# Kernel tuning notes

Measured on AMD Instinct MI355X. Metric: run time of the kernel, lower is better.

The kernel has to match this reference:

```python
import jax, jax.numpy as jnp
import numpy as np

D_MODEL, D_FF, D_NEURON, N_HEADS = 1024, 4096, 128, 8
HEAD_DIM = D_NEURON // N_HEADS
LN_EPS = 1e-5

def gelu(x):
    return jax.nn.gelu(x, approximate=False)  # torch default is exact erf GELU

def setup_inputs() -> dict:
    key = jax.random.key(0)
    ks = jax.random.split(key, 16)
    s = 0.02
    inp = {
        "x": jax.random.normal(ks[0], (2, 2048, D_MODEL), jnp.float32),
        "neuron_patterns": jax.random.normal(ks[1], (D_FF, D_MODEL), jnp.float32) * s,
        "neuron_vecs": jax.random.normal(ks[2], (D_FF, D_NEURON), jnp.float32) * s,
        "neuron_out_dirs": jax.random.normal(ks[3], (D_FF, D_MODEL), jnp.float32) * s,
        "router_w1": jax.random.normal(ks[4], (D_MODEL, D_MODEL), jnp.float32) * s,
        "router_w2": jax.random.normal(ks[5], (D_FF, D_MODEL), jnp.float32) * s,
        "ln_g": jnp.ones((D_MODEL,), jnp.float32),
        "ln_b": jnp.zeros((D_MODEL,), jnp.float32),
        "in_proj_w": jax.random.normal(ks[6], (3 * D_NEURON, D_NEURON), jnp.float32) * s,
        "in_proj_b": jnp.zeros((3 * D_NEURON,), jnp.float32),
        "out_proj_w": jax.random.normal(ks[7], (D_NEURON, D_NEURON), jnp.float32) * s,
        "out_proj_b": jnp.zeros((D_NEURON,), jnp.float32),
        "wp1_w": jax.random.normal(ks[8], (D_NEURON // 2, D_NEURON), jnp.float32) * s,
        "wp1_b": jnp.zeros((D_NEURON // 2,), jnp.float32),
        "wp2_w": jax.random.normal(ks[9], (1, D_NEURON // 2), jnp.float32) * s,
        "wp2_b": jnp.zeros((1,), jnp.float32),
        "top_k": 32,
    }
    return inp

def _forward(x, neuron_patterns, neuron_vecs, neuron_out_dirs, router_w1, router_w2,
             ln_g, ln_b, in_proj_w, in_proj_b, out_proj_w, out_proj_b,
             wp1_w, wp1_b, wp2_w, wp2_b, top_k):
    B, S, D = x.shape
    xf = x.reshape(-1, D)                                  # [N, D]
    # Router (MLP): LayerNorm -> gelu(x @ W1^T) -> @ W2^T
    mu = jnp.mean(xf, axis=-1, keepdims=True)
    var = jnp.mean(jnp.square(xf - mu), axis=-1, keepdims=True)
    xn = (xf - mu) * jax.lax.rsqrt(var + LN_EPS) * ln_g + ln_b
    h = gelu(xn @ router_w1.T)
    scores = h @ router_w2.T                               # [N, d_ff]
    _, idx = jax.lax.top_k(scores, top_k)                  # [N, k]
    pats = neuron_patterns[idx]                            # [N, k, D]
    sems = neuron_vecs[idx]                                # [N, k, dn]
    dirs = neuron_out_dirs[idx]                            # [N, k, D]
    base = gelu(jnp.einsum('nd,nkd->nk', xf, pats))        # [N, k]
    # Small self-attention over the k gathered neuron semantics (eval: no dropout)
    qkv = sems @ in_proj_w.T + in_proj_b                   # [N, k, 3*dn]
    q, kk, v = jnp.split(qkv, 3, axis=-1)
    N, K = q.shape[0], q.shape[1]
    q = q.reshape(N, K, N_HEADS, HEAD_DIM)
    kk = kk.reshape(N, K, N_HEADS, HEAD_DIM)
    v = v.reshape(N, K, N_HEADS, HEAD_DIM)
    att = jnp.einsum('nqhd,nkhd->nhqk', q, kk) / jnp.sqrt(jnp.float32(HEAD_DIM))
    att = jax.nn.softmax(att, axis=-1)
    ao = jnp.einsum('nhqk,nkhd->nqhd', att, v).reshape(N, K, D_NEURON)
    attended = ao @ out_proj_w.T + out_proj_b              # [N, k, dn]
    # Gate: sigmoid(MLP(attended)) -> [N, k, 1]
    sw = jax.nn.sigmoid(gelu(attended @ wp1_w.T + wp1_b) @ wp2_w.T + wp2_b)
    final = base[..., None] * sw                           # [N, k, 1]
    out = jnp.einsum('nko,nkd->nd', final, dirs)           # sum over k neurons
    return out.reshape(B, S, D)

def reference(x, neuron_patterns, neuron_vecs, neuron_out_dirs, router_w1, router_w2,
              ln_g, ln_b, in_proj_w, in_proj_b, out_proj_w, out_proj_b,
              wp1_w, wp1_b, wp2_w, wp2_b, top_k):
    return _forward(x, neuron_patterns, neuron_vecs, neuron_out_dirs, router_w1, router_w2,
                    ln_g, ln_b, in_proj_w, in_proj_b, out_proj_w, out_proj_b,
                    wp1_w, wp1_b, wp2_w, wp2_b, top_k)
```

## Files before the change

### kernel.cpp

```cpp
#include <hip/hip_runtime.h>
#include <math.h>

#define N_TOK 4096
#define DM 1024
#define DFF 4096
#define DN 128
#define NH 8
#define HD 16
#define KSEL 32
#define KCAND 48
#define KMAX 64

typedef __attribute__((ext_vector_type(4))) float floatx4;
typedef __attribute__((ext_vector_type(8))) short short8;
typedef __attribute__((ext_vector_type(8))) unsigned short ushort8v;
typedef __attribute__((ext_vector_type(4))) unsigned short ushort4v;

__device__ __forceinline__ float gelu_f(float x) {
  return 0.5f * x * (1.0f + erff(x * 0.70710678118654752440f));
}
__device__ __forceinline__ float bf2f(unsigned short u) {
  union { unsigned int i; float f; } v; v.i = ((unsigned int)u) << 16; return v.f;
}
__device__ __forceinline__ unsigned short f2bf(float f) {
  unsigned int x = __float_as_uint(f);
  unsigned int r = (x + 0x7fffu + ((x >> 16) & 1u)) >> 16;
  return (unsigned short)r;
}
__device__ __forceinline__ void split3(float v, unsigned short& h, unsigned short& m,
                                       unsigned short& lo) {
  h = f2bf(v);
  float r1 = v - bf2f(h);
  m = f2bf(r1);
  float r2 = r1 - bf2f(m);
  lo = f2bf(r2);
}

__global__ __launch_bounds__(256) void ln3_kernel(const float* __restrict__ x,
    const float* __restrict__ g, const float* __restrict__ b,
    unsigned short* __restrict__ xh, unsigned short* __restrict__ xm,
    unsigned short* __restrict__ xl) {
  int n = blockIdx.x, tid = threadIdx.x;
  const float* row = x + (size_t)n * DM;
  float s = 0.f, sq = 0.f;
  for (int i = tid; i < DM; i += 256) { float v = row[i]; s += v; sq += v * v; }
  for (int off = 32; off; off >>= 1) { s += __shfl_down(s, off); sq += __shfl_down(sq, off); }
  __shared__ float ss[4], ssq[4];
  __shared__ float s_mu, s_rs;
  int wid = tid >> 6;
  if ((tid & 63) == 0) { ss[wid] = s; ssq[wid] = sq; }
  __syncthreads();
  if (tid == 0) {
    float S = ss[0] + ss[1] + ss[2] + ss[3];
    float Q = ssq[0] + ssq[1] + ssq[2] + ssq[3];
    float mu = S * (1.f / DM);
    float var = Q * (1.f / DM) - mu * mu;
    s_mu = mu; s_rs = rsqrtf(var + 1e-5f);
  }
  __syncthreads();
  float mu = s_mu, rs = s_rs;
  size_t base = (size_t)n * DM;
  for (int i = tid; i < DM; i += 256) {
    float v = (row[i] - mu) * rs * g[i] + b[i];
    unsigned short h, m, lo;
    split3(v, h, m, lo);
    xh[base + i] = h; xm[base + i] = m; xl[base + i] = lo;
  }
}

__global__ __launch_bounds__(256) void prep_kernel(
    const float* __restrict__ rw2, unsigned short* __restrict__ w2b,
    const float* __restrict__ pats, unsigned short* __restrict__ patsb,
    const float* __restrict__ dirs, unsigned short* __restrict__ dirsb,
    const float* __restrict__ opw, unsigned short* __restrict__ opwb,
    const float* __restrict__ w1, unsigned short* __restrict__ w1b,
    const float* __restrict__ rw1, unsigned short* __restrict__ w1h,
    unsigned short* __restrict__ w1m, unsigned short* __restrict__ w1l) {
  int b = blockIdx.x, t = threadIdx.x;
  if (b < 12288) {
    const float* src; unsigned short* dst; int local;
    if (b < 4096) { src = rw2; dst = w2b; local = b; }
    else if (b < 8192) { src = pats; dst = patsb; local = b - 4096; }
    else { src = dirs; dst = dirsb; local = b - 8192; }
    int i = (local * 256 + t) * 4;
    float4 v = *(const float4*)(src + i);
    ushort4v o = {f2bf(v.x), f2bf(v.y), f2bf(v.z), f2bf(v.w)};
    *(ushort4v*)(dst + i) = o;
  } else if (b < 12304) {
    int i = ((b - 12288) * 256 + t) * 4;
    float4 v = *(const float4*)(opw + i);
    ushort4v o = {f2bf(v.x), f2bf(v.y), f2bf(v.z), f2bf(v.w)};
    *(ushort4v*)(opwb + i) = o;
  } else if (b < 12312) {
    int i = ((b - 12304) * 256 + t) * 4;
    float4 v = *(const float4*)(w1 + i);
    ushort4v o = {f2bf(v.x), f2bf(v.y), f2bf(v.z), f2bf(v.w)};
    *(ushort4v*)(w1b + i) = o;
  } else {
    int i = ((b - 12312) * 256 + t) * 4;
    float4 v = *(const float4*)(rw1 + i);
    unsigned short h0, m0, l0, h1, m1, l1, h2, m2, l2, h3, m3, l3;
    split3(v.x, h0, m0, l0);
    split3(v.y, h1, m1, l1);
    split3(v.z, h2, m2, l2);
    split3(v.w, h3, m3, l3);
    ushort4v hh = {h0, h1, h2, h3};
    ushort4v mm = {m0, m1, m2, m3};
    ushort4v ll = {l0, l1, l2, l3};
    *(ushort4v*)(w1h + i) = hh;
    *(ushort4v*)(w1m + i) = mm;
    *(ushort4v*)(w1l + i) = ll;
  }
}

__global__ __launch_bounds__(256) void gemm1s(
    const unsigned short* __restrict__ Ah_, const unsigned short* __restrict__ Am_,
    const unsigned short* __restrict__ Al_, const unsigned short* __restrict__ Bh_,
    const unsigned short* __restrict__ Bm_, const unsigned short* __restrict__ Bl_,
    float* __restrict__ H, unsigned short* __restrict__ Hb) {
  __shared__ short Ahs[64 * 32], Ams[64 * 32], Als[64 * 32];
  __shared__ short Bhs[64 * 32], Bms[64 * 32], Bls[64 * 32];
  const int K = 1024;
  const int N = DM;
  int tid = threadIdx.x;
  int w = tid >> 6, l = tid & 63;
  int wr = w >> 1, wc = w & 1;
  size_t brow = (size_t)blockIdx.y * 64;
  size_t bcol = (size_t)blockIdx.x * 64;

  int r0 = w * 16 + (l >> 2);
  int g0 = (l & 3) ^ ((r0 >> 1) & 3);
  size_t oA = (brow + r0) * (size_t)K + g0 * 8;
  size_t oB = (bcol + r0) * (size_t)K + g0 * 8;
  const short* gAh = (const short*)Ah_ + oA;
  const short* gAm = (const short*)Am_ + oA;
  const short* gAl = (const short*)Al_ + oA;
  const short* gBh = (const short*)Bh_ + oB;
  const short* gBm = (const short*)Bm_ + oB;
  const short* gBl = (const short*)Bl_ + oB;
  short* lAh = &Ahs[w * 512]; short* lAm = &Ams[w * 512]; short* lAl = &Als[w * 512];
  short* lBh = &Bhs[w * 512]; short* lBm = &Bms[w * 512]; short* lBl = &Bls[w * 512];

  const short8 *pah[2], *pam[2], *pal[2], *pbh[2], *pbm[2], *pbl[2];
#pragma unroll
  for (int i = 0; i < 2; i++) {
    int m = wr * 32 + i * 16 + (l & 15);
    int slot = m * 4 + ((l >> 4) ^ ((m >> 1) & 3));
    pah[i] = (const short8*)&Ahs[slot * 8];
    pam[i] = (const short8*)&Ams[slot * 8];
    pal[i] = (const short8*)&Als[slot * 8];
    int nn = wc * 32 + i * 16 + (l & 15);
    int slotb = nn * 4 + ((l >> 4) ^ ((nn >> 1) & 3));
    pbh[i] = (const short8*)&Bhs[slotb * 8];
    pbm[i] = (const short8*)&Bms[slotb * 8];
    pbl[i] = (const short8*)&Bls[slotb * 8];
  }

  floatx4 acc[2][2];
#pragma unroll
  for (int i = 0; i < 2; i++)
#pragma unroll
    for (int j = 0; j < 2; j++) acc[i][j] = (floatx4){0.f, 0.f, 0.f, 0.f};

#define GLD(GP, LB) \
  __builtin_amdgcn_global_load_lds((const __attribute__((address_space(1))) unsigned int*)(GP), \
                                   (__attribute__((address_space(3))) unsigned int*)(LB), 16, 0, 0)

  for (int k0 = 0; k0 < K; k0 += 32) {
    __syncthreads();
    GLD(gAh + k0, lAh); GLD(gAm + k0, lAm); GLD(gAl + k0, lAl);
    GLD(gBh + k0, lBh); GLD(gBm + k0, lBm); GLD(gBl + k0, lBl);
    __syncthreads();
    short8 ah[2], am[2], al[2], bh[2], bm[2], bl[2];
#pragma unroll
    for (int i = 0; i < 2; i++) {
      ah[i] = *pah[i]; am[i] = *pam[i]; al[i] = *pal[i];
      bh[i] = *pbh[i]; bm[i] = *pbm[i]; bl[i] = *pbl[i];
    }
#pragma unroll
    for (int i = 0; i < 2; i++)
#pragma unroll
      for (int j = 0; j < 2; j++)
        acc[i][j] = __builtin_amdgcn_mfma_f32_16x16x32_bf16(ah[i], bh[j], acc[i][j], 0, 0, 0);
#pragma unroll
    for (int i = 0; i < 2; i++)
#pragma unroll
      for (int j = 0; j < 2; j++)
        acc[i][j] = __builtin_amdgcn_mfma_f32_16x16x32_bf16(am[i], bh[j], acc[i][j], 0, 0, 0);
#pragma unroll
    for (int i = 0; i < 2; i++)
#pragma unroll
      for (int j = 0; j < 2; j++)
        acc[i][j] = __builtin_amdgcn_mfma_f32_16x16x32_bf16(ah[i], bm[j], acc[i][j], 0, 0, 0);
#pragma unroll
    for (int i = 0; i < 2; i++)
#pragma unroll
      for (int j = 0; j < 2; j++)
        acc[i][j] = __builtin_amdgcn_mfma_f32_16x16x32_bf16(al[i], bh[j], acc[i][j], 0, 0, 0);
#pragma unroll
    for (int i = 0; i < 2; i++)
#pragma unroll
      for (int j = 0; j < 2; j++)
        acc[i][j] = __builtin_amdgcn_mfma_f32_16x16x32_bf16(ah[i], bl[j], acc[i][j], 0, 0, 0);
#pragma unroll
    for (int i = 0; i < 2; i++)
#pragma unroll
      for (int j = 0; j < 2; j++)
        acc[i][j] = __builtin_amdgcn_mfma_f32_16x16x32_bf16(am[i], bm[j], acc[i][j], 0, 0, 0);
  }
#undef GLD

#pragma unroll
  for (int i = 0; i < 2; i++) {
#pragma unroll
    for (int j = 0; j < 2; j++) {
#pragma unroll
      for (int r = 0; r < 4; r++) {
        size_t row = brow + wr * 32 + i * 16 + (l >> 4) * 4 + r;
        size_t col = bcol + wc * 32 + j * 16 + (l & 15);
        float v = gelu_f(acc[i][j][r]);
        H[row * N + col] = v;
        Hb[row * N + col] = f2bf(v);
      }
    }
  }
}

__global__ __launch_bounds__(256) void gemm_bf(const unsigned short* __restrict__ Ah,
    const unsigned short* __restrict__ Bh, unsigned short* __restrict__ C) {
  __shared__ short Asd[128 * 32];
  __shared__ short Bsd[128 * 32];
  const int K = 1024;
  int tid = threadIdx.x;
  int w = tid >> 6, l = tid & 63;
  size_t brow = (size_t)blockIdx.y * 128;
  size_t bcol = (size_t)blockIdx.x * 128;
  const short* Ab = (const short*)Ah + brow * K;
  const short* Bb = (const short*)Bh + bcol * K;

  int r0 = w * 32 + (l >> 2);
  int g0 = (l & 3) ^ ((r0 >> 1) & 3);
  const short* Ag0 = Ab + (size_t)r0 * K + g0 * 8;
  const short* Ag1 = Ab + (size_t)(r0 + 16) * K + g0 * 8;
  const short* Bg0 = Bb + (size_t)r0 * K + g0 * 8;
  const short* Bg1 = Bb + (size_t)(r0 + 16) * K + g0 * 8;
  short* ALds0 = &Asd[w * 1024];
  short* ALds1 = &Asd[w * 1024 + 512];
  short* BLds0 = &Bsd[w * 1024];
  short* BLds1 = &Bsd[w * 1024 + 512];

  const short8* aptr[4];
  const short8* bptr[4];
#pragma unroll
  for (int i = 0; i < 4; i++) {
    int m = (w >> 1) * 64 + i * 16 + (l & 15);
    int slot = m * 4 + ((l >> 4) ^ ((m >> 1) & 3));
    aptr[i] = (const short8*)&Asd[slot * 8];
    int n = (w & 1) * 64 + i * 16 + (l & 15);
    int slotb = n * 4 + ((l >> 4) ^ ((n >> 1) & 3));
    bptr[i] = (const short8*)&Bsd[slotb * 8];
  }

  floatx4 acc[4][4];
#pragma unroll
  for (int i = 0; i < 4; i++)
#pragma unroll
    for (int j = 0; j < 4; j++) acc[i][j] = (floatx4){0.f, 0.f, 0.f, 0.f};

  for (int k0 = 0; k0 < K; k0 += 32) {
    __syncthreads();
    __builtin_amdgcn_global_load_lds((const __attribute__((address_space(1))) unsigned int*)(Ag0 + k0),
                                     (__attribute__((address_space(3))) unsigned int*)ALds0, 16, 0, 0);
    __builtin_amdgcn_global_load_lds((const __attribute__((address_space(1))) unsigned int*)(Ag1 + k0),
                                     (__attribute__((address_space(3))) unsigned int*)ALds1, 16, 0, 0);
    __builtin_amdgcn_global_load_lds((const __attribute__((address_space(1))) unsigned int*)(Bg0 + k0),
                                     (__attribute__((address_space(3))) unsigned int*)BLds0, 16, 0, 0);
    __builtin_amdgcn_global_load_lds((const __attribute__((address_space(1))) unsigned int*)(Bg1 + k0),
                                     (__attribute__((address_space(3))) unsigned int*)BLds1, 16, 0, 0);
    __syncthreads();
    short8 a[4], b[4];
#pragma unroll
    for (int i = 0; i < 4; i++) a[i] = *aptr[i];
#pragma unroll
    for (int j = 0; j < 4; j++) b[j] = *bptr[j];
#pragma unroll
    for (int i = 0; i < 4; i++)
#pragma unroll
      for (int j = 0; j < 4; j++)
        acc[i][j] = __builtin_amdgcn_mfma_f32_16x16x32_bf16(a[i], b[j], acc[i][j], 0, 0, 0);
  }

#pragma unroll
  for (int i = 0; i < 4; i++) {
#pragma unroll
    for (int j = 0; j < 4; j++) {
#pragma unroll
      for (int r = 0; r < 4; r++) {
        size_t row = brow + (w >> 1) * 64 + i * 16 + (l >> 4) * 4 + r;
        size_t col = bcol + (w & 1) * 64 + j * 16 + (l & 15);
        C[row * DFF + col] = f2bf(acc[i][j][r]);
      }
    }
  }
}

__global__ __launch_bounds__(256) void topk2_kernel(const unsigned short* __restrict__ scores,
    int* __restrict__ cand, int* __restrict__ cnt) {
  int wv = threadIdx.x >> 6, l = threadIdx.x & 63;
  int n = blockIdx.x * 4 + wv;
  const ushort8v* row = (const ushort8v*)(scores + (size_t)n * DFF);
  unsigned short key[64];
#pragma unroll
  for (int i = 0; i < 8; i++) {
    ushort8v v = row[l * 8 + i];
#pragma unroll
    for (int e = 0; e < 8; e++) {
      unsigned short u = v[e];
      key[i * 8 + e] = (u & 0x8000u) ? (unsigned short)(~u)
                                     : (unsigned short)(u | 0x8000u);
    }
  }
  unsigned int prefix = 0;
#pragma unroll
  for (int bit = 15; bit >= 0; bit--) {
    unsigned int probe = prefix | (1u << bit);
    int c = 0;
#pragma unroll
    for (int i = 0; i < 64; i++) c += (key[i] >= probe) ? 1 : 0;
#pragma unroll
    for (int s = 1; s < 64; s <<= 1) c += __shfl_xor(c, s);
    if (c >= KCAND) prefix = probe;
  }
  unsigned short thr = (unsigned short)prefix;
  unsigned long long ltmask = (1ull << l) - 1ull;
  int base = 0;
  int* outp = cand + (size_t)n * KMAX;
#pragma unroll
  for (int i = 0; i < 64; i++) {
    bool p = key[i] >= thr;
    unsigned long long m = __ballot(p);
    if (p) {
      int pos = base + __popcll(m & ltmask);
      if (pos < KMAX) outp[pos] = l * 64 + i;
    }
    base += __popcll(m);
  }
  if (l == 0) cnt[n] = base < KMAX ? base : KMAX;
}

__global__ __launch_bounds__(256) void rescore_kernel(const float* __restrict__ h,
    const float* __restrict__ w2f, const int* __restrict__ cand,
    const int* __restrict__ cnt, int* __restrict__ idx32) {
  __shared__ float sh[DM];
  __shared__ float sc[KMAX];
  __shared__ int sidx[KMAX];
  __shared__ int s_cnt;
  int n = blockIdx.x, tid = threadIdx.x;
  *(float4*)&sh[tid * 4] = *(const float4*)(h + (size_t)n * DM + tid * 4);
  if (tid == 0) s_cnt = cnt[n];
  if (tid < KMAX) { sidx[tid] = cand[(size_t)n * KMAX + tid]; sc[tid] = -INFINITY; }
  __syncthreads();
  int cntv = s_cnt;
  int w = tid >> 6, lane = tid & 63;
  for (int c = w; c < cntv; c += 4) {
    const float4* row = (const float4*)(w2f + (size_t)sidx[c] * DM);
    const float4* hp = (const float4*)sh;
    float s = 0.f;
#pragma unroll
    for (int t = 0; t < 4; t++) {
      float4 wv = row[t * 64 + lane];
      float4 hv = hp[t * 64 + lane];
      s = fmaf(wv.x, hv.x, s); s = fmaf(wv.y, hv.y, s);
      s = fmaf(wv.z, hv.z, s); s = fmaf(wv.w, hv.w, s);
    }
    for (int off = 32; off; off >>= 1) s += __shfl_xor(s, off);
    if (lane == 0) sc[c] = s;
  }
  __syncthreads();
  if (tid < cntv) {
    float st = sc[tid]; int it = sidx[tid];
    int rank = 0;
    for (int j = 0; j < KMAX; j++) {
      float sj = sc[j];
      rank += (sj > st) || (sj == st && sidx[j] < it);
    }
    if (rank < KSEL) idx32[(size_t)n * KSEL + rank] = it;
  }
}

__global__ __launch_bounds__(384) void qkvtab_kernel(const float* __restrict__ nv,
    const float* __restrict__ ipw, const float* __restrict__ ipb,
    unsigned short* __restrict__ tab) {
  __shared__ float s_nv[8 * 128];
  int f0 = blockIdx.x * 8;
  int tid = threadIdx.x;
  for (int i = tid; i < 8 * 128; i += 384) s_nv[i] = nv[(size_t)f0 * 128 + i];
  __syncthreads();
  int row = tid;
  float bias = ipb[row];
  float acc[8];
#pragma unroll
  for (int ff = 0; ff < 8; ff++) acc[ff] = bias;
  const float* wr = ipw + (size_t)row * 128;
  for (int c = 0; c < 128; c++) {
    float w = wr[c];
#pragma unroll
    for (int ff = 0; ff < 8; ff++) acc[ff] = fmaf(s_nv[ff * 128 + c], w, acc[ff]);
  }
#pragma unroll
  for (int ff = 0; ff < 8; ff++) tab[(size_t)(f0 + ff) * 384 + row] = f2bf(acc[ff]);
}

#define KVS 132
#define AOS 132
__global__ __launch_bounds__(256) void tail6_kernel(
    const float* __restrict__ xf, const unsigned short* __restrict__ pats_b,
    const unsigned short* __restrict__ dirs_b, const unsigned short* __restrict__ qtab_b,
    const int* __restrict__ idxs,
    const unsigned short* __restrict__ opwb, const float* __restrict__ opb,
    const unsigned short* __restrict__ w1b, const float* __restrict__ b1,
    const float* __restrict__ w2, const float* __restrict__ b2,
    float* __restrict__ out) {
  __shared__ float s_k[32 * KVS];
  __shared__ float s_v[32 * KVS];
  __shared__ float s_base[32];
  __shared__ float s_coef[32];
  __shared__ int s_idx[32];
  unsigned short* s_ao = (unsigned short*)s_k;
  unsigned short* s_at = (unsigned short*)s_v;

  int n = blockIdx.x, tid = threadIdx.x;
  int w = tid >> 6, l = tid & 63;

  if (tid < 32) s_idx[tid] = idxs[(size_t)n * 32 + tid];
  __syncthreads();

#pragma unroll
  for (int p = 0; p < 4; p++) {
    int i = p * 256 + tid;
    int j = i >> 5, c = i & 31;
    int half = c >> 4, cc = c & 15;
    ushort8v v = *(const ushort8v*)(qtab_b + (size_t)s_idx[j] * 384 + 128 + half * 128 + cc * 8);
    float4 f0 = {bf2f(v[0]), bf2f(v[1]), bf2f(v[2]), bf2f(v[3])};
    float4 f1 = {bf2f(v[4]), bf2f(v[5]), bf2f(v[6]), bf2f(v[7])};
    float* dst = (half ? s_v : s_k) + j * KVS + cc * 8;
    *(float4*)dst = f0;
    *(float4*)(dst + 4) = f1;
  }

  {
    int j = tid >> 3, g = tid & 7;
    const ushort8v* pr = (const ushort8v*)(pats_b + (size_t)s_idx[j] * DM);
    const float4* xr = (const float4*)(xf + (size_t)n * DM);
    float s = 0.f;
#pragma unroll 4
    for (int it = 0; it < 16; it++) {
      int ch = it * 8 + g;
      ushort8v pv = pr[ch];
      float4 xv0 = xr[ch * 2];
      float4 xv1 = xr[ch * 2 + 1];
      s = fmaf(bf2f(pv[0]), xv0.x, s); s = fmaf(bf2f(pv[1]), xv0.y, s);
      s = fmaf(bf2f(pv[2]), xv0.z, s); s = fmaf(bf2f(pv[3]), xv0.w, s);
      s = fmaf(bf2f(pv[4]), xv1.x, s); s = fmaf(bf2f(pv[5]), xv1.y, s);
      s = fmaf(bf2f(pv[6]), xv1.z, s); s = fmaf(bf2f(pv[7]), xv1.w, s);
    }
    s += __shfl_xor(s, 1);
    s += __shfl_xor(s, 2);
    s += __shfl_xor(s, 4);
    if (g == 0) s_base[j] = gelu_f(s);
  }
  __syncthreads();

  float att[32];
  int qj = l & 31;
  int h0 = w * 2 + (l >> 5);
  {
    const ushort8v* qr = (const ushort8v*)(qtab_b + (size_t)s_idx[qj] * 384 + h0 * 16);
    ushort8v q0 = qr[0], q1 = qr[1];
    float q[16];
#pragma unroll
    for (int e = 0; e < 8; e++) { q[e] = bf2f(q0[e]); q[8 + e] = bf2f(q1[e]); }
#pragma unroll 8
    for (int kj = 0; kj < 32; kj++) {
      const float4* kr = (const float4*)&s_k[kj * KVS + h0 * 16];
      float4 k0 = kr[0], k1 = kr[1], k2 = kr[2], k3 = kr[3];
      float s = 0.f;
      s = fmaf(q[0], k0.x, s);  s = fmaf(q[1], k0.y, s);
      s = fmaf(q[2], k0.z, s);  s = fmaf(q[3], k0.w, s);
      s = fmaf(q[4], k1.x, s);  s = fmaf(q[5], k1.y, s);
      s = fmaf(q[6], k1.z, s);  s = fmaf(q[7], k1.w, s);
      s = fmaf(q[8], k2.x, s);  s = fmaf(q[9], k2.y, s);
      s = fmaf(q[10], k2.z, s); s = fmaf(q[11], k2.w, s);
      s = fmaf(q[12], k3.x, s); s = fmaf(q[13], k3.y, s);
      s = fmaf(q[14], k3.z, s); s = fmaf(q[15], k3.w, s);
      att[kj] = s * 0.25f;
    }
    float m = att[0];
#pragma unroll
    for (int k = 1; k < 32; k++) m = fmaxf(m, att[k]);
    float sum = 0.f;
#pragma unroll
    for (int k = 0; k < 32; k++) { att[k] = expf(att[k] - m); sum += att[k]; }
    float inv = 1.f / sum;
#pragma unroll
    for (int k = 0; k < 32; k++) att[k] *= inv;
  }
  __syncthreads();

  {
    float o[16];
#pragma unroll
    for (int e = 0; e < 16; e++) o[e] = 0.f;
#pragma unroll 8
    for (int kj = 0; kj < 32; kj++) {
      const float4* vr = (const float4*)&s_v[kj * KVS + h0 * 16];
      float4 v0 = vr[0], v1 = vr[1], v2 = vr[2], v3 = vr[3];
      float a = att[kj];
      o[0] = fmaf(a, v0.x, o[0]);   o[1] = fmaf(a, v0.y, o[1]);
      o[2] = fmaf(a, v0.z, o[2]);   o[3] = fmaf(a, v0.w, o[3]);
      o[4] = fmaf(a, v1.x, o[4]);   o[5] = fmaf(a, v1.y, o[5]);
      o[6] = fmaf(a, v1.z, o[6]);   o[7] = fmaf(a, v1.w, o[7]);
      o[8] = fmaf(a, v2.x, o[8]);   o[9] = fmaf(a, v2.y, o[9]);
      o[10] = fmaf(a, v2.z, o[10]); o[11] = fmaf(a, v2.w, o[11]);
      o[12] = fmaf(a, v3.x, o[12]); o[13] = fmaf(a, v3.y, o[13]);
      o[14] = fmaf(a, v3.z, o[14]); o[15] = fmaf(a, v3.w, o[15]);
    }
    ushort8v o0, o1;
#pragma unroll
    for (int e = 0; e < 8; e++) { o0[e] = f2bf(o[e]); o1[e] = f2bf(o[8 + e]); }
    ushort8v* ao = (ushort8v*)&s_ao[qj * AOS + h0 * 16];
    ao[0] = o0; ao[1] = o1;
  }
  __syncthreads();

  {
    floatx4 acc[4];
#pragma unroll
    for (int nt = 0; nt < 4; nt++) acc[nt] = (floatx4){0.f, 0.f, 0.f, 0.f};
    int rbase = (w & 1) * 16;
    int cblk = (w >> 1) * 4;
#pragma unroll
    for (int kst = 0; kst < 4; kst++) {
      short8 a = *(const short8*)&s_ao[(rbase + (l & 15)) * AOS + kst * 32 + (l >> 4) * 8];
#pragma unroll
      for (int nt = 0; nt < 4; nt++) {
        short8 b = *(const short8*)&opwb[(size_t)((cblk + nt) * 16 + (l & 15)) * 128 + kst * 32 + (l >> 4) * 8];
        acc[nt] = __builtin_amdgcn_mfma_f32_16x16x32_bf16(a, b, acc[nt], 0, 0, 0);
      }
    }
#pragma unroll
    for (int nt = 0; nt < 4; nt++) {
      int col = (cblk + nt) * 16 + (l & 15);
      float bias = opb[col];
#pragma unroll
      for (int r = 0; r < 4; r++) {
        int row = rbase + (l >> 4) * 4 + r;
        s_at[row * AOS + col] = f2bf(acc[nt][r] + bias);
      }
    }
  }
  __syncthreads();

  if (w < 2) {
    floatx4 acc[4];
#pragma unroll
    for (int nt = 0; nt < 4; nt++) acc[nt] = (floatx4){0.f, 0.f, 0.f, 0.f};
#pragma unroll
    for (int kst = 0; kst < 4; kst++) {
      short8 a = *(const short8*)&s_at[(w * 16 + (l & 15)) * AOS + kst * 32 + (l >> 4) * 8];
#pragma unroll
      for (int nt = 0; nt < 4; nt++) {
        short8 b = *(const short8*)&w1b[(size_t)(nt * 16 + (l & 15)) * 128 + kst * 32 + (l >> 4) * 8];
        acc[nt] = __builtin_amdgcn_mfma_f32_16x16x32_bf16(a, b, acc[nt], 0, 0, 0);
      }
    }
    float p[4] = {0.f, 0.f, 0.f, 0.f};
#pragma unroll
    for (int nt = 0; nt < 4; nt++) {
      int col = nt * 16 + (l & 15);
      float bb = b1[col], ww = w2[col];
#pragma unroll
      for (int r = 0; r < 4; r++)
        p[r] = fmaf(gelu_f(acc[nt][r] + bb), ww, p[r]);
    }
#pragma unroll
    for (int r = 0; r < 4; r++) {
      p[r] += __shfl_xor(p[r], 1);
      p[r] += __shfl_xor(p[r], 2);
      p[r] += __shfl_xor(p[r], 4);
      p[r] += __shfl_xor(p[r], 8);
    }
    if ((l & 15) == 0) {
      float b2v = b2[0];
#pragma unroll
      for (int r = 0; r < 4; r++) {
        int row = w * 16 + (l >> 4) * 4 + r;
        float sw = 1.f / (1.f + expf(-(p[r] + b2v)));
        s_coef[row] = s_base[row] * sw;
      }
    }
  }
  __syncthreads();

  {
    int d0 = tid * 4;
    float4 a = {0.f, 0.f, 0.f, 0.f};
#pragma unroll 8
    for (int j = 0; j < 32; j++) {
      float c = s_coef[j];
      ushort4v dv = *(const ushort4v*)&dirs_b[(size_t)s_idx[j] * DM + d0];
      a.x = fmaf(c, bf2f(dv.x), a.x);
      a.y = fmaf(c, bf2f(dv.y), a.y);
      a.z = fmaf(c, bf2f(dv.z), a.z);
      a.w = fmaf(c, bf2f(dv.w), a.w);
    }
    *(float4*)&out[(size_t)n * 1024 + d0] = a;
  }
}

extern "C" void kernel_launch(void* const* d_in, const int* in_sizes, int n_in,
                              void* d_out, int out_size, void* d_ws, size_t ws_size,
                              hipStream_t stream) {
  const float* x    = (const float*)d_in[0];
  const float* pats = (const float*)d_in[1];
  const float* nv   = (const float*)d_in[2];
  const float* dirs = (const float*)d_in[3];
  const float* rw1  = (const float*)d_in[4];
  const float* rw2  = (const float*)d_in[5];
  const float* lng  = (const float*)d_in[6];
  const float* lnb  = (const float*)d_in[7];
  const float* ipw  = (const float*)d_in[8];
  const float* ipb  = (const float*)d_in[9];
  const float* opw  = (const float*)d_in[10];
  const float* opb  = (const float*)d_in[11];
  const float* w1   = (const float*)d_in[12];
  const float* b1   = (const float*)d_in[13];
  const float* w2   = (const float*)d_in[14];
  const float* b2   = (const float*)d_in[15];
  float* out = (float*)d_out;

  const size_t MB = 1u << 20;
  char* ws = (char*)d_ws;
  unsigned short* xnh  = (unsigned short*)(ws + 0);
  unsigned short* xnm  = (unsigned short*)(ws + 8 * MB);
  float* h             = (float*)(ws + 16 * MB);
  unsigned short* sb   = (unsigned short*)(ws + 32 * MB);
  unsigned short* w1h  = (unsigned short*)(ws + 32 * MB);
  unsigned short* w1m  = (unsigned short*)(ws + 34 * MB);
  unsigned short* w1l  = (unsigned short*)(ws + 36 * MB);
  unsigned short* xnl  = (unsigned short*)(ws + 38 * MB);
  unsigned short* qtab = (unsigned short*)(ws + 64 * MB);
  unsigned short* hb   = (unsigned short*)(ws + 67 * MB);
  unsigned short* w2b  = (unsigned short*)(ws + 75 * MB);
  unsigned short* patsb= (unsigned short*)(ws + 83 * MB);
  unsigned short* dirsb= (unsigned short*)(ws + 91 * MB);
  unsigned short* opwb = (unsigned short*)(ws + 99 * MB);
  unsigned short* w1b  = (unsigned short*)(ws + 99 * MB + 64 * 1024);
  int* idx32           = (int*)(ws + 100 * MB);
  int* cand            = (int*)(ws + 101 * MB);
  int* cnt             = (int*)(ws + 102 * MB);

  ln3_kernel<<<N_TOK, 256, 0, stream>>>(x, lng, lnb, xnh, xnm, xnl);
  prep_kernel<<<13336, 256, 0, stream>>>(rw2, w2b, pats, patsb, dirs, dirsb,
                                         opw, opwb, w1, w1b, rw1, w1h, w1m, w1l);
  gemm1s<<<dim3(DM / 64, N_TOK / 64), 256, 0, stream>>>(xnh, xnm, xnl, w1h, w1m, w1l, h, hb);
  gemm_bf<<<dim3(DFF / 128, N_TOK / 128), 256, 0, stream>>>(hb, w2b, sb);
  topk2_kernel<<<N_TOK / 4, 256, 0, stream>>>(sb, cand, cnt);
  rescore_kernel<<<N_TOK, 256, 0, stream>>>(h, rw2, cand, cnt, idx32);
  qkvtab_kernel<<<DFF / 8, 384, 0, stream>>>(nv, ipw, ipb, qtab);
  tail6_kernel<<<N_TOK, 256, 0, stream>>>(x, patsb, dirsb, qtab, idx32,
                                          opwb, opb, w1b, b1, w2, b2, out);
}
```

Baseline: 483.4 us.

## Compute per-token neuron attention with bf16 MFMA instead of scalar FMA

```diff
diff --git a/kernel.cpp b/kernel.cpp
--- a/kernel.cpp
+++ b/kernel.cpp
@@ -411,9 +411,10 @@
   for (int ff = 0; ff < 8; ff++) tab[(size_t)(f0 + ff) * 384 + row] = f2bf(acc[ff]);
 }
 
-#define KVS 132
+#define KS 132
+#define VTS 36
 #define AOS 132
-__global__ __launch_bounds__(256) void tail6_kernel(
+__global__ __launch_bounds__(256) void tail8_kernel(
     const float* __restrict__ xf, const unsigned short* __restrict__ pats_b,
     const unsigned short* __restrict__ dirs_b, const unsigned short* __restrict__ qtab_b,
     const int* __restrict__ idxs,
@@ -421,41 +422,40 @@
     const unsigned short* __restrict__ w1b, const float* __restrict__ b1,
     const float* __restrict__ w2, const float* __restrict__ b2,
     float* __restrict__ out) {
-  __shared__ float s_k[32 * KVS];
-  __shared__ float s_v[32 * KVS];
+  __shared__ unsigned short s_k[32 * KS];
+  __shared__ unsigned short s_vt[128 * VTS];
   __shared__ float s_base[32];
   __shared__ float s_coef[32];
   __shared__ int s_idx[32];
-  unsigned short* s_ao = (unsigned short*)s_k;
-  unsigned short* s_at = (unsigned short*)s_v;
+  unsigned short* s_ao = s_k;
+  unsigned short* s_at = s_vt;
 
   int n = blockIdx.x, tid = threadIdx.x;
   int w = tid >> 6, l = tid & 63;
+  int g = l >> 4, lc = l & 15;
 
   if (tid < 32) s_idx[tid] = idxs[(size_t)n * 32 + tid];
   __syncthreads();
 
 #pragma unroll
-  for (int p = 0; p < 4; p++) {
+  for (int p = 0; p < 2; p++) {
     int i = p * 256 + tid;
-    int j = i >> 5, c = i & 31;
-    int half = c >> 4, cc = c & 15;
-    ushort8v v = *(const ushort8v*)(qtab_b + (size_t)s_idx[j] * 384 + 128 + half * 128 + cc * 8);
-    float4 f0 = {bf2f(v[0]), bf2f(v[1]), bf2f(v[2]), bf2f(v[3])};
-    float4 f1 = {bf2f(v[4]), bf2f(v[5]), bf2f(v[6]), bf2f(v[7])};
-    float* dst = (half ? s_v : s_k) + j * KVS + cc * 8;
-    *(float4*)dst = f0;
-    *(float4*)(dst + 4) = f1;
+    int j = i >> 4, cc = i & 15;
+    ushort8v kv = *(const ushort8v*)(qtab_b + (size_t)s_idx[j] * 384 + 128 + cc * 8);
+    *(ushort8v*)&s_k[j * KS + cc * 8] = kv;
+    ushort8v vv = *(const ushort8v*)(qtab_b + (size_t)s_idx[j] * 384 + 256 + cc * 8);
+#pragma unroll
+    for (int e = 0; e < 8; e++) s_vt[(cc * 8 + e) * VTS + j] = vv[e];
   }
 
   {
-    int j = tid >> 3, g = tid & 7;
+    int j = tid >> 3, gq = tid & 7;
     const ushort8v* pr = (const ushort8v*)(pats_b + (size_t)s_idx[j] * DM);
     const float4* xr = (const float4*)(xf + (size_t)n * DM);
     float s = 0.f;
 #pragma unroll 4
     for (int it = 0; it < 16; it++) {
-      int ch = it * 8 + g;
+      int ch = it * 8 + gq;
       ushort8v pv = pr[ch];
       float4 xv0 = xr[ch * 2];
       float4 xv1 = xr[ch * 2 + 1];
@@ -467,69 +467,95 @@
     s += __shfl_xor(s, 1);
     s += __shfl_xor(s, 2);
     s += __shfl_xor(s, 4);
-    if (g == 0) s_base[j] = gelu_f(s);
-  }
-  __syncthreads();
-
-  float att[32];
-  int qj = l & 31;
-  int h0 = w * 2 + (l >> 5);
+    if (gq == 0) s_base[j] = gelu_f(s);
+  }
+  __syncthreads();
+
+  short8 pB[2][2];
   {
-    const ushort8v* qr = (const ushort8v*)(qtab_b + (size_t)s_idx[qj] * 384 + h0 * 16);
-    ushort8v q0 = qr[0], q1 = qr[1];
-    float q[16];
-#pragma unroll
-    for (int e = 0; e < 8; e++) { q[e] = bf2f(q0[e]); q[8 + e] = bf2f(q1[e]); }
-#pragma unroll 8
-    for (int kj = 0; kj < 32; kj++) {
-      const float4* kr = (const float4*)&s_k[kj * KVS + h0 * 16];
-      float4 k0 = kr[0], k1 = kr[1], k2 = kr[2], k3 = kr[3];
-      float s = 0.f;
-      s = fmaf(q[0], k0.x, s);  s = fmaf(q[1], k0.y, s);
-      s = fmaf(q[2], k0.z, s);  s = fmaf(q[3], k0.w, s);
-      s = fmaf(q[4], k1.x, s);  s = fmaf(q[5], k1.y, s);
-      s = fmaf(q[6], k1.z, s);  s = fmaf(q[7], k1.w, s);
-      s = fmaf(q[8], k2.x, s);  s = fmaf(q[9], k2.y, s);
-      s = fmaf(q[10], k2.z, s); s = fmaf(q[11], k2.w, s);
-      s = fmaf(q[12], k3.x, s); s = fmaf(q[13], k3.y, s);
-      s = fmaf(q[14], k3.z, s); s = fmaf(q[15], k3.w, s);
-      att[kj] = s * 0.25f;
-    }
-    float m = att[0];
-#pragma unroll
-    for (int k = 1; k < 32; k++) m = fmaxf(m, att[k]);
-    float sum = 0.f;
-#pragma unroll
-    for (int k = 0; k < 32; k++) { att[k] = expf(att[k] - m); sum += att[k]; }
-    float inv = 1.f / sum;
-#pragma unroll
-    for (int k = 0; k < 32; k++) att[k] *= inv;
+    short8 zero8 = {0, 0, 0, 0, 0, 0, 0, 0};
+    int srcA = (((2 * g) & 3) << 4) | lc;
+    int srcB = (((2 * g + 1) & 3) << 4) | lc;
+    bool hiSel = (g >= 2);
+#pragma unroll
+    for (int hh = 0; hh < 2; hh++) {
+      int h = w * 2 + hh;
+      short8 qf[2], kf[2];
+#pragma unroll
+      for (int qt = 0; qt < 2; qt++) {
+        short8 q = zero8;
+        if (g < 2) q = *(const short8*)(qtab_b + (size_t)s_idx[qt * 16 + lc] * 384 + h * 16 + g * 8);
+        qf[qt] = q;
+      }
+#pragma unroll
+      for (int kt = 0; kt < 2; kt++) {
+        short8 k = zero8;
+        if (g < 2) k = *(const short8*)&s_k[(kt * 16 + lc) * KS + h * 16 + g * 8];
+        kf[kt] = k;
+      }
+      floatx4 c[2][2];
+#pragma unroll
+      for (int kt = 0; kt < 2; kt++)
+#pragma unroll
+        for (int qt = 0; qt < 2; qt++)
+          c[kt][qt] = __builtin_amdgcn_mfma_f32_16x16x32_bf16(kf[kt], qf[qt],
+                                                              (floatx4){0.f, 0.f, 0.f, 0.f}, 0, 0, 0);
+#pragma unroll
+      for (int qt = 0; qt < 2; qt++) {
+        float v0[4], v1[4];
+#pragma unroll
+        for (int r = 0; r < 4; r++) { v0[r] = c[0][qt][r] * 0.25f; v1[r] = c[1][qt][r] * 0.25f; }
+        float m = v0[0];
+#pragma unroll
+        for (int r = 1; r < 4; r++) m = fmaxf(m, v0[r]);
+#pragma unroll
+        for (int r = 0; r < 4; r++) m = fmaxf(m, v1[r]);
+        m = fmaxf(m, __shfl_xor(m, 16));
+        m = fmaxf(m, __shfl_xor(m, 32));
+        float sum = 0.f;
+#pragma unroll
+        for (int r = 0; r < 4; r++) { v0[r] = expf(v0[r] - m); sum += v0[r]; }
+#pragma unroll
+        for (int r = 0; r < 4; r++) { v1[r] = expf(v1[r] - m); sum += v1[r]; }
+        sum += __shfl_xor(sum, 16);
+        sum += __shfl_xor(sum, 32);
+        float inv = 1.f / sum;
+        unsigned int u00 = ((unsigned int)f2bf(v0[1] * inv) << 16) | f2bf(v0[0] * inv);
+        unsigned int u01 = ((unsigned int)f2bf(v0[3] * inv) << 16) | f2bf(v0[2] * inv);
+        unsigned int u10 = ((unsigned int)f2bf(v1[1] * inv) << 16) | f2bf(v1[0] * inv);
+        unsigned int u11 = ((unsigned int)f2bf(v1[3] * inv) << 16) | f2bf(v1[2] * inv);
+        unsigned int a00 = (unsigned int)__shfl((int)u00, srcA);
+        unsigned int a01 = (unsigned int)__shfl((int)u01, srcA);
+        unsigned int a10 = (unsigned int)__shfl((int)u10, srcA);
+        unsigned int a11 = (unsigned int)__shfl((int)u11, srcA);
+        unsigned int b00 = (unsigned int)__shfl((int)u00, srcB);
+        unsigned int b01 = (unsigned int)__shfl((int)u01, srcB);
+        unsigned int b10 = (unsigned int)__shfl((int)u10, srcB);
+        unsigned int b11 = (unsigned int)__shfl((int)u11, srcB);
+        union { unsigned int u[4]; short8 s; } pb;
+        pb.u[0] = hiSel ? a10 : a00;
+        pb.u[1] = hiSel ? a11 : a01;
+        pb.u[2] = hiSel ? b10 : b00;
+        pb.u[3] = hiSel ? b11 : b01;
+        pB[hh][qt] = pb.s;
+      }
+    }
   }
   __syncthreads();
 
   {
-    float o[16];
-#pragma unroll
-    for (int e = 0; e < 16; e++) o[e] = 0.f;
-#pragma unroll 8
-    for (int kj = 0; kj < 32; kj++) {
-      const float4* vr = (const float4*)&s_v[kj * KVS + h0 * 16];
-      float4 v0 = vr[0], v1 = vr[1], v2 = vr[2], v3 = vr[3];
-      float a = att[kj];
-      o[0] = fmaf(a, v0.x, o[0]);   o[1] = fmaf(a, v0.y, o[1]);
-      o[2] = fmaf(a, v0.z, o[2]);   o[3] = fmaf(a, v0.w, o[3]);
-      o[4] = fmaf(a, v1.x, o[4]);   o[5] = fmaf(a, v1.y, o[5]);
-      o[6] = fmaf(a, v1.z, o[6]);   o[7] = fmaf(a, v1.w, o[7]);
-      o[8] = fmaf(a, v2.x, o[8]);   o[9] = fmaf(a, v2.y, o[9]);
-      o[10] = fmaf(a, v2.z, o[10]); o[11] = fmaf(a, v2.w, o[11]);
-      o[12] = fmaf(a, v3.x, o[12]); o[13] = fmaf(a, v3.y, o[13]);
-      o[14] = fmaf(a, v3.z, o[14]); o[15] = fmaf(a, v3.w, o[15]);
-    }
-    ushort8v o0, o1;
-#pragma unroll
-    for (int e = 0; e < 8; e++) { o0[e] = f2bf(o[e]); o1[e] = f2bf(o[8 + e]); }
-    ushort8v* ao = (ushort8v*)&s_ao[qj * AOS + h0 * 16];
-    ao[0] = o0; ao[1] = o1;
+#pragma unroll
+    for (int hh = 0; hh < 2; hh++) {
+      int h = w * 2 + hh;
+      short8 vtf = *(const short8*)&s_vt[(h * 16 + lc) * VTS + g * 8];
+#pragma unroll
+      for (int qt = 0; qt < 2; qt++) {
+        floatx4 o = __builtin_amdgcn_mfma_f32_16x16x32_bf16(vtf, pB[hh][qt],
+                                                            (floatx4){0.f, 0.f, 0.f, 0.f}, 0, 0, 0);
+        ushort4v ov = {f2bf(o[0]), f2bf(o[1]), f2bf(o[2]), f2bf(o[3])};
+        *(ushort4v*)&s_ao[(qt * 16 + lc) * AOS + h * 16 + g * 4] = ov;
+      }
+    }
   }
   __syncthreads();
 
@@ -541,20 +567,20 @@
     int cblk = (w >> 1) * 4;
 #pragma unroll
     for (int kst = 0; kst < 4; kst++) {
-      short8 a = *(const short8*)&s_ao[(rbase + (l & 15)) * AOS + kst * 32 + (l >> 4) * 8];
+      short8 a = *(const short8*)&s_ao[(rbase + lc) * AOS + kst * 32 + g * 8];
 #pragma unroll
       for (int nt = 0; nt < 4; nt++) {
-        short8 b = *(const short8*)&opwb[(size_t)((cblk + nt) * 16 + (l & 15)) * 128 + kst * 32 + (l >> 4) * 8];
+        short8 b = *(const short8*)&opwb[(size_t)((cblk + nt) * 16 + lc) * 128 + kst * 32 + g * 8];
         acc[nt] = __builtin_amdgcn_mfma_f32_16x16x32_bf16(a, b, acc[nt], 0, 0, 0);
       }
     }
 #pragma unroll
     for (int nt = 0; nt < 4; nt++) {
-      int col = (cblk + nt) * 16 + (l & 15);
+      int col = (cblk + nt) * 16 + lc;
       float bias = opb[col];
 #pragma unroll
       for (int r = 0; r < 4; r++) {
-        int row = rbase + (l >> 4) * 4 + r;
+        int row = rbase + g * 4 + r;
         s_at[row * AOS + col] = f2bf(acc[nt][r] + bias);
       }
     }
@@ -567,17 +593,17 @@
     for (int nt = 0; nt < 4; nt++) acc[nt] = (floatx4){0.f, 0.f, 0.f, 0.f};
 #pragma unroll
     for (int kst = 0; kst < 4; kst++) {
-      short8 a = *(const short8*)&s_at[(w * 16 + (l & 15)) * AOS + kst * 32 + (l >> 4) * 8];
+      short8 a = *(const short8*)&s_at[(w * 16 + lc) * AOS + kst * 32 + g * 8];
 #pragma unroll
       for (int nt = 0; nt < 4; nt++) {
-        short8 b = *(const short8*)&w1b[(size_t)(nt * 16 + (l & 15)) * 128 + kst * 32 + (l >> 4) * 8];
+        short8 b = *(const short8*)&w1b[(size_t)(nt * 16 + lc) * 128 + kst * 32 + g * 8];
         acc[nt] = __builtin_amdgcn_mfma_f32_16x16x32_bf16(a, b, acc[nt], 0, 0, 0);
       }
     }
     float p[4] = {0.f, 0.f, 0.f, 0.f};
 #pragma unroll
     for (int nt = 0; nt < 4; nt++) {
-      int col = nt * 16 + (l & 15);
+      int col = nt * 16 + lc;
       float bb = b1[col], ww = w2[col];
 #pragma unroll
       for (int r = 0; r < 4; r++)
@@ -590,11 +616,11 @@
       p[r] += __shfl_xor(p[r], 4);
       p[r] += __shfl_xor(p[r], 8);
     }
-    if ((l & 15) == 0) {
+    if (lc == 0) {
       float b2v = b2[0];
 #pragma unroll
       for (int r = 0; r < 4; r++) {
-        int row = w * 16 + (l >> 4) * 4 + r;
+        int row = w * 16 + g * 4 + r;
         float sw = 1.f / (1.f + expf(-(p[r] + b2v)));
         s_coef[row] = s_base[row] * sw;
       }
@@ -668,6 +694,6 @@
   topk2_kernel<<<N_TOK / 4, 256, 0, stream>>>(sb, cand, cnt);
   rescore_kernel<<<N_TOK, 256, 0, stream>>>(h, rw2, cand, cnt, idx32);
   qkvtab_kernel<<<DFF / 8, 384, 0, stream>>>(nv, ipw, ipb, qtab);
-  tail6_kernel<<<N_TOK, 256, 0, stream>>>(x, patsb, dirsb, qtab, idx32,
+  tail8_kernel<<<N_TOK, 256, 0, stream>>>(x, patsb, dirsb, qtab, idx32,
                                           opwb, opb, w1b, b1, w2, b2, out);
 }
```

New measurement: 469.1 us. -3.0%, faster.
